# Kernel tuning notes

Measured on AMD Instinct MI355X. Metric: run time of the kernel, lower is better.

## Reference

```python
import jax, jax.numpy as jnp
import numpy as np

ANCHORS = np.array([[116.0, 90.0], [156.0, 198.0], [373.0, 326.0]], dtype=np.float32)
NUM_CLASSES = 11
INPUT_SIZE = 1024
NA = 3
LAMBDA_COORD = 100.0
LAMBDA_NOOBJ = 0.5
IGNORE_THRES = 0.5  # only affects conf_mask, which is unused by the loss


def _wh_iou(gw, gh, anchors):
    # IoU of (0,0,gw,gh) vs (0,0,aw,ah): intersection = min of widths * min of heights
    inter = jnp.minimum(gw, anchors[:, 0]) * jnp.minimum(gh, anchors[:, 1])
    union = gw * gh + anchors[:, 0] * anchors[:, 1] - inter
    return inter / (union + 1e-16)


def _center_iou(gt, boxes):
    # gt: (4,) [cx,cy,w,h]; boxes: (nA,4) [cx,cy,w,h]
    g_x1, g_x2 = gt[0] - gt[2] / 2, gt[0] + gt[2] / 2
    g_y1, g_y2 = gt[1] - gt[3] / 2, gt[1] + gt[3] / 2
    b_x1, b_x2 = boxes[:, 0] - boxes[:, 2] / 2, boxes[:, 0] + boxes[:, 2] / 2
    b_y1, b_y2 = boxes[:, 1] - boxes[:, 3] / 2, boxes[:, 1] + boxes[:, 3] / 2
    iw = jnp.clip(jnp.minimum(g_x2, b_x2) - jnp.maximum(g_x1, b_x1), 0.0)
    ih = jnp.clip(jnp.minimum(g_y2, b_y2) - jnp.maximum(g_y1, b_y1), 0.0)
    inter = iw * ih
    union = gt[2] * gt[3] + boxes[:, 2] * boxes[:, 3] - inter
    return inter / (union + 1e-16)


def build_targets(pred_boxes, targets, scaled_anchors, dim):
    # Sequential scan over flattened (batch, target) pairs to preserve the
    # original scatter-overwrite semantics of the nested Python loops.
    nB, nT, _ = targets.shape
    f32 = jnp.float32
    z = jnp.zeros((nB, NA, dim, dim), f32)
    tcls0 = jnp.zeros((nB, NA, dim, dim, NUM_CLASSES), f32)
    bidx = jnp.repeat(jnp.arange(nB), nT)
    flat = targets.reshape(nB * nT, 5)
    arangeA = jnp.arange(NA)

    def step(carry, inp):
        mask, tx, ty, tw, th, tconf, tcls, nGT, nCorrect = carry
        b, tgt = inp
        valid = tgt.sum() != 0
        gx, gy = tgt[1] * dim, tgt[2] * dim
        gw, gh = tgt[3] * dim, tgt[4] * dim
        gi = gx.astype(jnp.int32)
        gj = gy.astype(jnp.int32)
        ious = _wh_iou(gw, gh, scaled_anchors)
        over = ious > 0.3
        sel = jnp.where(over.any(), over, arangeA == jnp.argmax(ious)) & valid  # (nA,)

        def upd(a, vals):
            old = a[b, :, gj, gi]
            return a.at[b, :, gj, gi].set(jnp.where(sel, vals, old))

        mask = upd(mask, 1.0)
        tconf = upd(tconf, 1.0)
        tx = upd(tx, gx - gi.astype(f32))
        ty = upd(ty, gy - gj.astype(f32))
        tw = upd(tw, jnp.log(gw / scaled_anchors[:, 0] + 1e-16))
        th = upd(th, jnp.log(gh / scaled_anchors[:, 1] + 1e-16))
        cls = tgt[0].astype(jnp.int32)
        old_c = tcls[b, :, gj, gi, cls]
        tcls = tcls.at[b, :, gj, gi, cls].set(jnp.where(sel, 1.0, old_c))
        # recall bookkeeping
        pb = pred_boxes[b, :, gj, gi, :]  # (nA,4)
        iou = _center_iou(jnp.stack([gx, gy, gw, gh]), pb)
        nGT = nGT + valid.astype(jnp.int32)
        nCorrect = nCorrect + jnp.any((iou > 0.5) & sel).astype(jnp.int32)
        return (mask, tx, ty, tw, th, tconf, tcls, nGT, nCorrect), None

    init = (z, z, z, z, z, z, tcls0, jnp.int32(0), jnp.int32(0))
    carry, _ = jax.lax.scan(step, init, (bidx, flat))
    return carry


def reference(x, targets):
    bs, _, g, _ = x.shape
    stride = float(INPUT_SIZE) / float(g)
    battrs = 5 + NUM_CLASSES
    pred = x.reshape(bs, NA, battrs, g, g).transpose(0, 1, 3, 4, 2)  # [B,A,H,W,16]
    px = jax.nn.sigmoid(pred[..., 0])
    py = jax.nn.sigmoid(pred[..., 1])
    pw = pred[..., 2]
    ph = pred[..., 3]
    conf = jax.nn.sigmoid(pred[..., 4])
    pred_cls = jax.nn.softmax(pred[..., 5:], axis=-1)  # softmax overwrites sigmoid in the original

    grid = jnp.arange(g, dtype=jnp.float32)
    grid_x = grid[None, None, None, :]
    grid_y = grid[None, None, :, None]
    sa = jnp.asarray(ANCHORS) / stride
    aw = sa[:, 0][None, :, None, None]
    ah = sa[:, 1][None, :, None, None]
    pred_boxes = jax.lax.stop_gradient(
        jnp.stack([px + grid_x + 0 * py, py + grid_y + 0 * px,
                   jnp.exp(pw) * aw + 0 * pw, jnp.exp(ph) * ah + 0 * ph], axis=-1))

    mask, tx, ty, tw, th, tconf, tcls, nGT, nCorrect = build_targets(pred_boxes, targets, sa, g)

    sq = lambda a, b: jnp.sum((a - b) ** 2)
    loss_x = LAMBDA_COORD * sq(px * mask, tx * mask)
    loss_y = LAMBDA_COORD * sq(py * mask, ty * mask)
    loss_w = LAMBDA_COORD * sq(pw * mask, tw * mask)
    loss_h = LAMBDA_COORD * sq(ph * mask, th * mask)
    loss_conf = sq(conf * tconf, tconf)
    loss_conf_no = LAMBDA_NOOBJ * sq(conf * (1 - tconf), tconf * (1 - tconf))
    cls_mask = mask[..., None]
    p = pred_cls * cls_mask
    t = tcls * cls_mask
    # torch BCELoss clamps log terms at -100
    logp = jnp.maximum(jnp.log(p), -100.0)
    log1mp = jnp.maximum(jnp.log(1.0 - p), -100.0)
    loss_cls = -jnp.sum(t * logp + (1.0 - t) * log1mp)
    loss = loss_x + loss_y + loss_w + loss_h + loss_conf + loss_cls + loss_conf_no
    recall = jnp.where(nGT > 0, nCorrect.astype(jnp.float32) / jnp.maximum(nGT, 1).astype(jnp.float32), 1.0)
    return (loss, loss_x, loss_y, loss_w, loss_h, loss_conf, loss_conf_no, loss_cls, recall)


def setup_inputs() -> dict:
    key = jax.random.key(0)
    k1, k2, k3, k4 = jax.random.split(key, 4)
    x = jax.random.normal(k1, (16, 48, 128, 128), dtype=jnp.float32)
    cls = jax.random.randint(k2, (16, 50, 1), 0, NUM_CLASSES).astype(jnp.float32)
    cxy = jax.random.uniform(k3, (16, 50, 2), minval=0.02, maxval=0.98)
    wh = jax.random.uniform(k4, (16, 50, 2), minval=0.02, maxval=0.30)
    targets = jnp.concatenate([cls, cxy, wh], axis=-1)
    # zero-pad last 10 GT slots per image (skipped by the sum==0 check)
    targets = targets * (jnp.arange(50) < 40)[None, :, None]
    return {"x": x, "targets": targets.astype(jnp.float32)}
```

## Files before the change

### kernel.cpp

```cpp
#include <hip/hip_runtime.h>

#define NBATCH 16
#define NT     50
#define GDIM   128
#define NC     11
#define PLANE  (GDIM * GDIM)
#define CONF_BLOCKS 192
#define TGT_BLOCKS  16
#define TOTAL_BLOCKS (1 + CONF_BLOCKS + TGT_BLOCKS)
#define TPB 256
#define NSLOTS (CONF_BLOCKS + TGT_BLOCKS * 9)
#define MAGIC32 0x7FC0DEADu

__device__ __forceinline__ float sigm(float x) { return 1.0f / (1.0f + expf(-x)); }

__device__ __forceinline__ void put_slot(unsigned long long* slot, float v) {
    unsigned long long pk = ((unsigned long long)MAGIC32 << 32) |
                            (unsigned long long)__float_as_uint(v);
    __hip_atomic_store(slot, pk, __ATOMIC_RELAXED, __HIP_MEMORY_SCOPE_AGENT);
}

struct TInfo {
    int gi, gj, cls, selm;
    float gx, gy, gw, gh;
};

__device__ __forceinline__ TInfo tinfo(const float* tg) {
    TInfo r;
    float c0 = tg[0], cx = tg[1], cy = tg[2], cw = tg[3], ch = tg[4];
    bool valid = ((c0 + cx + cy + cw + ch) != 0.0f);
    r.gx = cx * (float)GDIM;  r.gy = cy * (float)GDIM;
    r.gw = cw * (float)GDIM;  r.gh = ch * (float)GDIM;
    r.gi = (int)r.gx;  r.gj = (int)r.gy;
    r.cls = (int)c0;
    const float aw[3] = {14.5f, 19.5f, 46.625f};
    const float ah[3] = {11.25f, 24.75f, 40.75f};
    int selm = 0; float best = -1.0f; int bi = 0;
    #pragma unroll
    for (int a = 0; a < 3; a++) {
        float inter = fminf(r.gw, aw[a]) * fminf(r.gh, ah[a]);
        float uni   = r.gw * r.gh + aw[a] * ah[a] - inter;
        float iou   = inter / (uni + 1e-16f);
        if (iou > 0.3f) selm |= (1 << a);
        if (iou > best) { best = iou; bi = a; }
    }
    if (selm == 0) selm = (1 << bi);
    if (!valid) selm = 0;
    r.selm = selm;
    return r;
}

__global__ __launch_bounds__(TPB) void k_fused(const float* __restrict__ X,
                                               const float* __restrict__ T,
                                               float* __restrict__ ws,
                                               float* __restrict__ out) {
    const int bid = blockIdx.x, tid = threadIdx.x;
    unsigned long long* slots = (unsigned long long*)ws;

    if (bid == 0) {
        __shared__ float st[TGT_BLOCKS * 9];
        __shared__ float sf[9];
        __shared__ float sredc[4];
        float cv = 0.0f;
        for (int i = tid; i < NSLOTS; i += TPB) {
            unsigned long long v;
            for (;;) {
                v = __hip_atomic_load(&slots[i], __ATOMIC_RELAXED,
                                      __HIP_MEMORY_SCOPE_AGENT);
                if ((unsigned)(v >> 32) == MAGIC32) break;
                __builtin_amdgcn_s_sleep(1);
            }
            float val = __uint_as_float((unsigned)v);
            if (i < CONF_BLOCKS) cv += val;
            else st[i - CONF_BLOCKS] = val;
        }
        __syncthreads();
        #pragma unroll
        for (int o = 32; o > 0; o >>= 1) cv += __shfl_down(cv, o);
        if ((tid & 63) == 0) sredc[tid >> 6] = cv;
        if (tid < 9) {
            float fc = 0.0f;
            #pragma unroll
            for (int b = 0; b < TGT_BLOCKS; b++) fc += st[b * 9 + tid];
            sf[tid] = fc;
        }
        __syncthreads();
        if (tid == 0) {
            float f[9];
            #pragma unroll
            for (int c = 0; c < 9; c++) f[c] = sf[c];
            f[5] += sredc[0] + sredc[1] + sredc[2] + sredc[3];
            float total = f[0] + f[1] + f[2] + f[3] + f[4] + f[6] + f[5];
            out[0] = total;
            out[1] = f[0]; out[2] = f[1]; out[3] = f[2]; out[4] = f[3];
            out[5] = f[4]; out[6] = f[5]; out[7] = f[6];
            float nGT = f[7], nCorr = f[8];
            out[8] = (nGT > 0.0f) ? (nCorr / fmaxf(nGT, 1.0f)) : 1.0f;
        }
        return;
    }

    if (bid <= CONF_BLOCKS) {
        __shared__ float sred[4];
        const float4* X4 = reinterpret_cast<const float4*>(X);
        int cb = bid - 1;
        int p = cb >> 2, q = cb & 3;
        int bb = p / 3, a = p - bb * 3;
        int base4 = (bb * 48 + a * 16 + 4) * 4096 + q * 1024;
        float s = 0.0f;
        #pragma unroll
        for (int k = 0; k < 4; k++) {
            float4 v = X4[base4 + k * 256 + tid];
            float c0 = sigm(v.x), c1 = sigm(v.y), c2 = sigm(v.z), c3 = sigm(v.w);
            s += c0 * c0 + c1 * c1 + c2 * c2 + c3 * c3;
        }
        #pragma unroll
        for (int o = 32; o > 0; o >>= 1) s += __shfl_down(s, o);
        if ((tid & 63) == 0) sred[tid >> 6] = s;
        __syncthreads();
        if (tid == 0)
            put_slot(&slots[cb], 0.5f * (sred[0] + sred[1] + sred[2] + sred[3]));
        return;
    }

    __shared__ float stg[NT * 5];
    __shared__ int   pk[NT];
    __shared__ int   sanyv[NT * 3];
    __shared__ float sred[4][9];
    int b = bid - 1 - CONF_BLOCKS;
    for (int i = tid; i < NT * 5; i += TPB) stg[i] = T[b * NT * 5 + i];
    __syncthreads();

    TInfo me; me.selm = 0;
    int t = 0, a = 0;
    if (tid < NT * 3) {
        t = tid / 3; a = tid - t * 3;
        me = tinfo(stg + t * 5);
        if (a == 0) pk[t] = me.gi | (me.gj << 7) | (me.selm << 14) | (me.cls << 17);
    }
    __syncthreads();

    float res[9] = {0, 0, 0, 0, 0, 0, 0, 0, 0};
    int anyv = 0;
    bool selA = (tid < NT * 3) && ((me.selm >> a) & 1);
    if (selA) {
        int mykey = me.gi | (me.gj << 7);
        int lat = 0, clsba = 0;
        for (int e = 0; e < NT; e++) {
            int o = pk[e];
            if (((o >> (14 + a)) & 1) && ((o & 0x3FFF) == mykey)) {
                clsba |= 1 << ((o >> 17) & 0xF);
                if (e > t) lat = 1;
            }
        }
        float awa = (a == 0) ? 14.5f  : (a == 1) ? 19.5f  : 46.625f;
        float aha = (a == 0) ? 11.25f : (a == 1) ? 24.75f : 40.75f;
        int base = (b * 48 + a * 16) * PLANE + me.gj * GDIM + me.gi;
        float x0 = X[base];
        float x1 = X[base + PLANE];
        float x2 = X[base + 2 * PLANE];
        float x3 = X[base + 3 * PLANE];
        float g_x1 = me.gx - me.gw * 0.5f, g_x2 = me.gx + me.gw * 0.5f;
        float g_y1 = me.gy - me.gh * 0.5f, g_y2 = me.gy + me.gh * 0.5f;
        float bx = sigm(x0) + (float)me.gi;
        float by = sigm(x1) + (float)me.gj;
        float bw = expf(x2) * awa;
        float bh = expf(x3) * aha;
        float iw = fmaxf(fminf(g_x2, bx + bw * 0.5f) - fmaxf(g_x1, bx - bw * 0.5f), 0.0f);
        float ih = fmaxf(fminf(g_y2, by + bh * 0.5f) - fmaxf(g_y1, by - bh * 0.5f), 0.0f);
        float inter = iw * ih;
        float iou = inter / (me.gw * me.gh + bw * bh - inter + 1e-16f);
        anyv = (iou > 0.5f) ? 1 : 0;

        if (!lat) {
            float conf = sigm(X[base + 4 * PLANE]);
            float px = sigm(x0), py = sigm(x1);
            float txv = me.gx - (float)me.gi;
            float tyv = me.gy - (float)me.gj;
            float twv = logf(me.gw / awa + 1e-16f);
            float thv = logf(me.gh / aha + 1e-16f);
            res[0] = 100.0f * (px - txv) * (px - txv);
            res[1] = 100.0f * (py - tyv) * (py - tyv);
            res[2] = 100.0f * (x2 - twv) * (x2 - twv);
            res[3] = 100.0f * (x3 - thv) * (x3 - thv);
            res[4] = (conf - 1.0f) * (conf - 1.0f);
            res[5] = -0.5f * conf * conf;
            float l[NC]; float mx = -1e30f;
            #pragma unroll
            for (int c = 0; c < NC; c++) {
                l[c] = X[base + (5 + c) * PLANE];
                mx = fmaxf(mx, l[c]);
            }
            float S = 0.0f;
            #pragma unroll
            for (int c = 0; c < NC; c++) { l[c] = expf(l[c] - mx); S += l[c]; }
            float invS = 1.0f / S;
            float lcls = 0.0f;
            #pragma unroll
            for (int c = 0; c < NC; c++) {
                float p = l[c] * invS;
                float term = ((clsba >> c) & 1) ? fmaxf(logf(p), -100.0f)
                                                : fmaxf(logf(1.0f - p), -100.0f);
                lcls -= term;
            }
            res[6] = lcls;
        }
    }
    if (tid < NT * 3) sanyv[tid] = anyv;
    if (tid < NT * 3 && a == 0 && me.selm) res[7] = 1.0f;
    __syncthreads();
    if (tid < NT * 3 && a == 0 && me.selm)
        res[8] = (sanyv[tid] | sanyv[tid + 1] | sanyv[tid + 2]) ? 1.0f : 0.0f;

    #pragma unroll
    for (int o = 32; o > 0; o >>= 1) {
        #pragma unroll
        for (int c = 0; c < 9; c++) res[c] += __shfl_down(res[c], o);
    }
    if ((tid & 63) == 0) {
        #pragma unroll
        for (int c = 0; c < 9; c++) sred[tid >> 6][c] = res[c];
    }
    __syncthreads();
    if (tid == 0) {
        #pragma unroll
        for (int c = 0; c < 9; c++)
            put_slot(&slots[CONF_BLOCKS + b * 9 + c],
                     sred[0][c] + sred[1][c] + sred[2][c] + sred[3][c]);
    }
}

extern "C" void kernel_launch(void* const* d_in, const int* in_sizes, int n_in,
                              void* d_out, int out_size, void* d_ws, size_t ws_size,
                              hipStream_t stream) {
    const float* X = (const float*)d_in[0];
    const float* T = (const float*)d_in[1];
    float* out = (float*)d_out;
    float* wsf = (float*)d_ws;

    k_fused<<<TOTAL_BLOCKS, TPB, 0, stream>>>(X, T, wsf, out);
}
```

Measured before the change: 11.63 us.

## Publish per-wave partials and prefetch target-cell loads before block barrier

Conf and target blocks now write one slot per wavefront instead of reducing through shared memory and a __syncthreads, so the final block polls four times as many slots. Target blocks read their 5 target floats straight from global memory instead of staging them in shared memory, which removes one barrier. All 16 X values for a selected cell are loaded before the barrier so their latency overlaps the pk table construction. The cost is more slot polling and more live registers in the target path.

```diff
diff --git a/kernel.cpp b/kernel.cpp
--- a/kernel.cpp
+++ b/kernel.cpp
@@ -9,7 +9,9 @@
 #define TGT_BLOCKS  16
 #define TOTAL_BLOCKS (1 + CONF_BLOCKS + TGT_BLOCKS)
 #define TPB 256
-#define NSLOTS (CONF_BLOCKS + TGT_BLOCKS * 9)
+#define NCONF_SLOTS (CONF_BLOCKS * 4)
+#define NTGT_SLOTS  (TGT_BLOCKS * 4 * 9)
+#define NSLOTS (NCONF_SLOTS + NTGT_SLOTS)
 #define MAGIC32 0x7FC0DEADu
 
 __device__ __forceinline__ float sigm(float x) { return 1.0f / (1.0f + expf(-x)); }
@@ -18,6 +20,16 @@
     unsigned long long pk = ((unsigned long long)MAGIC32 << 32) |
                             (unsigned long long)__float_as_uint(v);
     __hip_atomic_store(slot, pk, __ATOMIC_RELAXED, __HIP_MEMORY_SCOPE_AGENT);
+}
+
+__device__ __forceinline__ float poll_slot(const unsigned long long* slot) {
+    unsigned long long v;
+    for (;;) {
+        v = __hip_atomic_load(slot, __ATOMIC_RELAXED, __HIP_MEMORY_SCOPE_AGENT);
+        if ((unsigned)(v >> 32) == MAGIC32) break;
+        __builtin_amdgcn_s_sleep(1);
+    }
+    return __uint_as_float((unsigned)v);
 }
 
 struct TInfo {
@@ -58,30 +70,19 @@
     unsigned long long* slots = (unsigned long long*)ws;
 
     if (bid == 0) {
-        __shared__ float st[TGT_BLOCKS * 9];
+        __shared__ float st[NTGT_SLOTS];
         __shared__ float sf[9];
         __shared__ float sredc[4];
         float cv = 0.0f;
-        for (int i = tid; i < NSLOTS; i += TPB) {
-            unsigned long long v;
-            for (;;) {
-                v = __hip_atomic_load(&slots[i], __ATOMIC_RELAXED,
-                                      __HIP_MEMORY_SCOPE_AGENT);
-                if ((unsigned)(v >> 32) == MAGIC32) break;
-                __builtin_amdgcn_s_sleep(1);
-            }
-            float val = __uint_as_float((unsigned)v);
-            if (i < CONF_BLOCKS) cv += val;
-            else st[i - CONF_BLOCKS] = val;
-        }
+        for (int i = tid; i < NCONF_SLOTS; i += TPB) cv += poll_slot(&slots[i]);
+        for (int i = tid; i < NTGT_SLOTS; i += TPB) st[i] = poll_slot(&slots[NCONF_SLOTS + i]);
         __syncthreads();
         #pragma unroll
         for (int o = 32; o > 0; o >>= 1) cv += __shfl_down(cv, o);
         if ((tid & 63) == 0) sredc[tid >> 6] = cv;
         if (tid < 9) {
             float fc = 0.0f;
-            #pragma unroll
-            for (int b = 0; b < TGT_BLOCKS; b++) fc += st[b * 9 + tid];
+            for (int w = 0; w < TGT_BLOCKS * 4; w++) fc += st[w * 9 + tid];
             sf[tid] = fc;
         }
         __syncthreads();
@@ -101,12 +102,11 @@
     }
 
     if (bid <= CONF_BLOCKS) {
-        __shared__ float sred[4];
         const float4* X4 = reinterpret_cast<const float4*>(X);
         int cb = bid - 1;
         int p = cb >> 2, q = cb & 3;
-        int bb = p / 3, a = p - bb * 3;
-        int base4 = (bb * 48 + a * 16 + 4) * 4096 + q * 1024;
+        int bb = p / 3, aa = p - bb * 3;
+        int base4 = (bb * 48 + aa * 16 + 4) * 4096 + q * 1024;
         float s = 0.0f;
         #pragma unroll
         for (int k = 0; k < 4; k++) {
@@ -116,33 +116,43 @@
         }
         #pragma unroll
         for (int o = 32; o > 0; o >>= 1) s += __shfl_down(s, o);
-        if ((tid & 63) == 0) sred[tid >> 6] = s;
-        __syncthreads();
-        if (tid == 0)
-            put_slot(&slots[cb], 0.5f * (sred[0] + sred[1] + sred[2] + sred[3]));
+        if ((tid & 63) == 0)
+            put_slot(&slots[cb * 4 + (tid >> 6)], 0.5f * s);
         return;
     }
 
-    __shared__ float stg[NT * 5];
-    __shared__ int   pk[NT];
-    __shared__ int   sanyv[NT * 3];
-    __shared__ float sred[4][9];
+    __shared__ int pk[NT];
+    __shared__ int sanyv[NT * 3];
     int b = bid - 1 - CONF_BLOCKS;
-    for (int i = tid; i < NT * 5; i += TPB) stg[i] = T[b * NT * 5 + i];
-    __syncthreads();
 
     TInfo me; me.selm = 0;
     int t = 0, a = 0;
     if (tid < NT * 3) {
         t = tid / 3; a = tid - t * 3;
-        me = tinfo(stg + t * 5);
+        const float* tp = T + b * NT * 5 + t * 5;
+        float tg5[5] = {tp[0], tp[1], tp[2], tp[3], tp[4]};
+        me = tinfo(tg5);
         if (a == 0) pk[t] = me.gi | (me.gj << 7) | (me.selm << 14) | (me.cls << 17);
+    }
+    bool selA = (tid < NT * 3) && ((me.selm >> a) & 1);
+
+    float x0 = 0, x1 = 0, x2 = 0, x3 = 0, cf = 0, l[NC];
+    float awa = (a == 0) ? 14.5f  : (a == 1) ? 19.5f  : 46.625f;
+    float aha = (a == 0) ? 11.25f : (a == 1) ? 24.75f : 40.75f;
+    if (selA) {
+        int base = (b * 48 + a * 16) * PLANE + me.gj * GDIM + me.gi;
+        x0 = X[base];
+        x1 = X[base + PLANE];
+        x2 = X[base + 2 * PLANE];
+        x3 = X[base + 3 * PLANE];
+        cf = X[base + 4 * PLANE];
+        #pragma unroll
+        for (int c = 0; c < NC; c++) l[c] = X[base + (5 + c) * PLANE];
     }
     __syncthreads();
 
     float res[9] = {0, 0, 0, 0, 0, 0, 0, 0, 0};
     int anyv = 0;
-    bool selA = (tid < NT * 3) && ((me.selm >> a) & 1);
     if (selA) {
         int mykey = me.gi | (me.gj << 7);
         int lat = 0, clsba = 0;
@@ -153,13 +163,6 @@
                 if (e > t) lat = 1;
             }
         }
-        float awa = (a == 0) ? 14.5f  : (a == 1) ? 19.5f  : 46.625f;
-        float aha = (a == 0) ? 11.25f : (a == 1) ? 24.75f : 40.75f;
-        int base = (b * 48 + a * 16) * PLANE + me.gj * GDIM + me.gi;
-        float x0 = X[base];
-        float x1 = X[base + PLANE];
-        float x2 = X[base + 2 * PLANE];
-        float x3 = X[base + 3 * PLANE];
         float g_x1 = me.gx - me.gw * 0.5f, g_x2 = me.gx + me.gw * 0.5f;
         float g_y1 = me.gy - me.gh * 0.5f, g_y2 = me.gy + me.gh * 0.5f;
         float bx = sigm(x0) + (float)me.gi;
@@ -173,7 +176,7 @@
         anyv = (iou > 0.5f) ? 1 : 0;
 
         if (!lat) {
-            float conf = sigm(X[base + 4 * PLANE]);
+            float conf = sigm(cf);
             float px = sigm(x0), py = sigm(x1);
             float txv = me.gx - (float)me.gi;
             float tyv = me.gy - (float)me.gj;
@@ -185,12 +188,9 @@
             res[3] = 100.0f * (x3 - thv) * (x3 - thv);
             res[4] = (conf - 1.0f) * (conf - 1.0f);
             res[5] = -0.5f * conf * conf;
-            float l[NC]; float mx = -1e30f;
-            #pragma unroll
-            for (int c = 0; c < NC; c++) {
-                l[c] = X[base + (5 + c) * PLANE];
-                mx = fmaxf(mx, l[c]);
-            }
+            float mx = -1e30f;
+            #pragma unroll
+            for (int c = 0; c < NC; c++) mx = fmaxf(mx, l[c]);
             float S = 0.0f;
             #pragma unroll
             for (int c = 0; c < NC; c++) { l[c] = expf(l[c] - mx); S += l[c]; }
@@ -218,15 +218,10 @@
         for (int c = 0; c < 9; c++) res[c] += __shfl_down(res[c], o);
     }
     if ((tid & 63) == 0) {
-        #pragma unroll
-        for (int c = 0; c < 9; c++) sred[tid >> 6][c] = res[c];
-    }
-    __syncthreads();
-    if (tid == 0) {
+        int w = tid >> 6;
         #pragma unroll
         for (int c = 0; c < 9; c++)
-            put_slot(&slots[CONF_BLOCKS + b * 9 + c],
-                     sred[0][c] + sred[1][c] + sred[2][c] + sred[3][c]);
+            put_slot(&slots[NCONF_SLOTS + (b * 4 + w) * 9 + c], res[c]);
     }
 }
 
```

Result: no change. 11.54 us (-0.8%).
